# Performance work log

Hardware: AMD Instinct MI355X
Metric: run time of the kernel (lower is better)

## Reference

```python
import jax, jax.numpy as jnp
import numpy as np

H = 2048          # hidden_size
NH = 16           # num_attention_heads
D_NOPE = 64
D_ROPE = 64
D_V = 64
KV_RANK = 256
E = 8             # n_routed_experts
INTER = 1408      # moe_intermediate_size
EPS = 1e-6
THETA = 10000.0
B, S = 1, 2048
Q_HEAD = D_NOPE + D_ROPE


def rms_norm(x, w, eps=EPS):
    xf = x.astype(jnp.float32)
    var = jnp.mean(xf * xf, axis=-1, keepdims=True)
    return (w * (xf * jax.lax.rsqrt(var + eps))).astype(x.dtype)


def rotate_half(x):
    d = x.shape[-1] // 2
    return jnp.concatenate([-x[..., d:], x[..., :d]], axis=-1)


def rope_tables(seq_len, dim, theta=THETA):
    inv_freq = 1.0 / (theta ** (jnp.arange(0, dim, 2, dtype=jnp.float32) / dim))
    t = jnp.arange(seq_len, dtype=jnp.float32)
    freqs = jnp.outer(t, inv_freq)
    emb = jnp.concatenate([freqs, freqs], axis=-1)  # [S, dim]
    return jnp.cos(emb), jnp.sin(emb)


def setup_inputs() -> dict:
    key = jax.random.key(0)
    ks = jax.random.split(key, 10)
    sc = 0.02
    inp = {
        "positions": jnp.broadcast_to(jnp.arange(S, dtype=jnp.int32)[None, :], (B, S)),
        "hidden_states": jax.random.normal(ks[0], (B, S, H), dtype=jnp.float32),
        "input_ln_w": jnp.ones((H,), jnp.float32),
        "q_proj_w": jax.random.normal(ks[1], (NH * Q_HEAD, H), jnp.float32) * sc,
        "kv_a_w": jax.random.normal(ks[2], (KV_RANK + D_ROPE, H), jnp.float32) * sc,
        "kv_a_ln_w": jnp.ones((KV_RANK,), jnp.float32),
        "kv_b_w": jax.random.normal(ks[3], (NH * (D_NOPE + D_V), KV_RANK), jnp.float32) * sc,
        "o_proj_w": jax.random.normal(ks[4], (H, NH * D_V), jnp.float32) * sc,
        "post_ln_w": jnp.ones((H,), jnp.float32),
        "gate_w": jax.random.normal(ks[5], (E, H), jnp.float32) * sc,
        "fc1_w": jax.random.normal(ks[6], (E, INTER, H), jnp.float32) * sc,
        "fc2_w": jax.random.normal(ks[7], (E, H, INTER), jnp.float32) * sc,
    }
    return inp


def reference(positions, hidden_states, input_ln_w, q_proj_w, kv_a_w, kv_a_ln_w,
              kv_b_w, o_proj_w, post_ln_w, gate_w, fc1_w, fc2_w):
    x = hidden_states
    sa_in = rms_norm(x, input_ln_w)

    # Q projection -> [B, NH, S, D_NOPE + D_ROPE]
    q = (sa_in @ q_proj_w.T).reshape(B, S, NH, Q_HEAD).transpose(0, 2, 1, 3)
    q_nope, q_pe = q[..., :D_NOPE], q[..., D_NOPE:]

    # KV compression path
    ckv_pe = sa_in @ kv_a_w.T                       # [B, S, KV_RANK + D_ROPE]
    compressed_kv, k_pe = ckv_pe[..., :KV_RANK], ckv_pe[..., KV_RANK:]
    k_pe = k_pe.reshape(B, S, 1, D_ROPE).transpose(0, 2, 1, 3)  # [B,1,S,Dr]
    kv = (rms_norm(compressed_kv, kv_a_ln_w) @ kv_b_w.T)
    kv = kv.reshape(B, S, NH, D_NOPE + D_V).transpose(0, 2, 1, 3)
    k_nope, v = kv[..., :D_NOPE], kv[..., D_NOPE:]

    # RoPE on pe halves
    cos, sin = rope_tables(S, D_ROPE)
    cos_sel = cos[positions][:, None]               # [B,1,S,Dr]
    sin_sel = sin[positions][:, None]
    q_pe = q_pe * cos_sel + rotate_half(q_pe) * sin_sel
    k_pe = k_pe * cos_sel + rotate_half(k_pe) * sin_sel

    query = jnp.concatenate([q_nope, q_pe], axis=-1)                       # [B,NH,S,Dq]
    key = jnp.concatenate([k_nope, jnp.broadcast_to(k_pe, (B, NH, S, D_ROPE))], axis=-1)

    scale = Q_HEAD ** -0.5
    scores = jnp.einsum("bhqd,bhkd->bhqk", query, key) * scale
    causal = jnp.tril(jnp.ones((S, S), dtype=bool))
    scores = jnp.where(causal, scores, jnp.finfo(scores.dtype).min)
    attn = jax.nn.softmax(scores, axis=-1)
    ctx = jnp.einsum("bhqk,bhkd->bhqd", attn, v)                            # [B,NH,S,Dv]
    ctx = ctx.transpose(0, 2, 1, 3).reshape(B, S, NH * D_V)
    attn_out = ctx @ o_proj_w.T

    x = x + attn_out

    # dense all-expert MoE
    mlp_in = rms_norm(x, post_ln_w)
    probs = jax.nn.softmax(mlp_in @ gate_w.T, axis=-1)                      # [B,S,E]
    h = jax.nn.silu(jnp.einsum("bsd,eid->bsei", mlp_in, fc1_w))             # [B,S,E,INTER]
    moe_out = jnp.einsum("bse,bsei,ehi->bsh", probs, h, fc2_w)

    return x + moe_out
```

## Files before the change

### kernel.cpp

```cpp
#include <hip/hip_runtime.h>
#include <cstdint>
#include <cstddef>

typedef __bf16 bf16;
typedef __bf16 bf16x8 __attribute__((ext_vector_type(8)));
typedef float  f32x4  __attribute__((ext_vector_type(4)));

constexpr int S_      = 2048;
constexpr int H_      = 2048;
constexpr int NH_     = 16;
constexpr int KV_RANK_= 256;
constexpr int EXP_    = 8;
constexpr int INTER_  = 1408;
constexpr int QH_     = 128;
constexpr float EPS_  = 1e-6f;

__device__ inline void gload16(const void* g, void* l) {
  __builtin_amdgcn_global_load_lds(
      (const __attribute__((address_space(1))) void*)g,
      (__attribute__((address_space(3))) void*)l, 16, 0, 0);
}

enum { EPI_BF16 = 0, EPI_F32 = 1, EPI_ADD = 2, EPI_SILU = 3, EPI_ATOM = 4 };

template <int EPI, typename TB, int TILE>
__global__ void __launch_bounds__(256, 3) gemm_bt(
    const bf16* __restrict__ A, const TB* __restrict__ B,
    void* __restrict__ Cv, const float* __restrict__ aux,
    int M, int N, int K, int lda, int ldb, int ldc,
    long zA, long zB, long zC, long auxZ, int auxRS,
    int kPerE, long bExpStride, int expBasePerZ)
{
  constexpr int FR = TILE / 32;
  const int tileN = blockIdx.x * TILE;
  const int tileM = blockIdx.y * TILE;
  const int z = blockIdx.z;
  A += (long)z * zA;

  __shared__ __align__(16) bf16 As[TILE * 64];
  __shared__ __align__(16) TB   Bs[TILE * 64];
  char* AsB = (char*)As;
  char* BsB = (char*)Bs;

  const int tid  = threadIdx.x;
  const int lane = tid & 63;
  const int wave = tid >> 6;
  const int wr = wave >> 1, wc = wave & 1;
  const int quad = lane >> 4, r16 = lane & 15;

  const int ldbe = (kPerE > 0) ? kPerE : ldb;
  const TB* BzBase = (kPerE > 0) ? (B + (long)z * expBasePerZ * bExpStride)
                                 : (B + (long)z * zB);

  constexpr int IA = TILE / 32;
  const bf16* aG[IA]; char* aL[IA];
#pragma unroll
  for (int i = 0; i < IA; i++) {
    int n = (wave * IA + i) * 64 + lane;
    int row = n >> 3, cp = n & 7;
    int cc = (cp ^ (row & 7)) << 3;
    int rowg = tileM + row; if (rowg > M - 1) rowg = M - 1;
    aG[i] = A + (long)rowg * lda + cc;
    aL[i] = AsB + (long)(wave * IA + i) * 1024;
  }
  constexpr int IB = (sizeof(TB) == 4) ? (TILE / 16) : (TILE / 32);
  const TB* bG[IB]; char* bL[IB];
#pragma unroll
  for (int i = 0; i < IB; i++) {
    int n = (wave * IB + i) * 64 + lane;
    int row, cc;
    if constexpr (sizeof(TB) == 4) { row = n >> 4; cc = ((n & 15) ^ (row & 15)) << 2; }
    else                           { row = n >> 3; cc = ((n & 7)  ^ (row & 7))  << 3; }
    int rowg = tileN + row; if (rowg > N - 1) rowg = N - 1;
    bG[i] = BzBase + (long)rowg * ldbe + cc;
    bL[i] = BsB + (long)(wave * IB + i) * 1024;
  }

  int aOff[FR], bOff[FR];
#pragma unroll
  for (int i = 0; i < FR; i++) {
    int row = wr * (TILE / 2) + i * 16 + r16;
    aOff[i] = row * 128 + ((quad ^ (row & 7)) << 4);
  }
#pragma unroll
  for (int j = 0; j < FR; j++) {
    int row = wc * (TILE / 2) + j * 16 + r16;
    if constexpr (sizeof(TB) == 4) bOff[j] = row * 256 + (((2 * quad) ^ (row & 15)) << 4);
    else                           bOff[j] = row * 128 + ((quad ^ (row & 7)) << 4);
  }

  f32x4 acc[FR][FR];
#pragma unroll
  for (int i = 0; i < FR; i++)
#pragma unroll
    for (int j = 0; j < FR; j++)
#pragma unroll
      for (int r = 0; r < 4; r++) acc[i][j][r] = 0.f;

  int bk = 0; long eOff = 0;
  for (int k0 = 0; k0 < K; k0 += 64) {
#pragma unroll
    for (int i = 0; i < IA; i++) gload16(aG[i] + k0, aL[i]);
#pragma unroll
    for (int i = 0; i < IB; i++) gload16(bG[i] + eOff + bk, bL[i]);
    __syncthreads();

#pragma unroll
    for (int s = 0; s < 2; s++) {
      bf16x8 af[FR], bfv[FR];
#pragma unroll
      for (int i = 0; i < FR; i++)
        af[i] = *(const bf16x8*)(AsB + (aOff[i] ^ (s << 6)));
#pragma unroll
      for (int j = 0; j < FR; j++) {
        if constexpr (sizeof(TB) == 2) {
          bfv[j] = *(const bf16x8*)(BsB + (bOff[j] ^ (s << 6)));
        } else {
          int a0 = bOff[j] ^ (s << 7);
          f32x4 lo = *(const f32x4*)(BsB + a0);
          f32x4 hi = *(const f32x4*)(BsB + (a0 ^ 16));
          bf16x8 v;
          v[0]=(bf16)lo[0]; v[1]=(bf16)lo[1]; v[2]=(bf16)lo[2]; v[3]=(bf16)lo[3];
          v[4]=(bf16)hi[0]; v[5]=(bf16)hi[1]; v[6]=(bf16)hi[2]; v[7]=(bf16)hi[3];
          bfv[j] = v;
        }
      }
#pragma unroll
      for (int i = 0; i < FR; i++)
#pragma unroll
        for (int j = 0; j < FR; j++)
          acc[i][j] = __builtin_amdgcn_mfma_f32_16x16x32_bf16(af[i], bfv[j], acc[i][j], 0, 0, 0);
    }
    __syncthreads();

    bk += 64;
    if (kPerE > 0 && bk >= kPerE) { bk = 0; eOff += bExpStride; }
  }

  bf16*  Cb = (bf16*)Cv + (long)z * zC;
  float* Cf = (float*)Cv + (long)z * zC;
  const float* auxp = aux + (long)z * auxZ;
  const int mB = tileM + wr * (TILE / 2) + quad * 4;
  const int nB = tileN + wc * (TILE / 2) + r16;
#pragma unroll
  for (int i = 0; i < FR; i++) {
#pragma unroll
    for (int r = 0; r < 4; r++) {
      int gm = mB + i * 16 + r;
      if (gm >= M) continue;
      float rowAux = 0.f;
      if constexpr (EPI == EPI_SILU) rowAux = auxp[(long)gm * auxRS];
#pragma unroll
      for (int j = 0; j < FR; j++) {
        int gn = nB + j * 16;
        if (gn >= N) continue;
        float v = acc[i][j][r];
        long off = (long)gm * ldc + gn;
        if constexpr (EPI == EPI_BF16)      Cb[off] = (bf16)v;
        else if constexpr (EPI == EPI_F32)  Cf[off] = v;
        else if constexpr (EPI == EPI_ADD)  Cf[off] = auxp[(long)gm * auxRS + gn] + v;
        else if constexpr (EPI == EPI_SILU) { float sv = v / (1.f + __expf(-v)); Cb[off] = (bf16)(sv * rowAux); }
        else                                atomicAdd(&Cf[off], v);
      }
    }
  }
}

__global__ void __launch_bounds__(256) flash_k(
    const bf16* __restrict__ q, const bf16* __restrict__ k,
    const bf16* __restrict__ vt, bf16* __restrict__ ctx, float scale)
{
  const int h  = blockIdx.x;
  const int qt = (int)gridDim.y - 1 - (int)blockIdx.y;
  const int tid = threadIdx.x, lane = tid & 63, wave = tid >> 6;
  const int quad = lane >> 4, r16 = lane & 15;

  __shared__ __align__(16) bf16 Ks[64 * 128];
  __shared__ __align__(16) bf16 Vs[64 * 64];
  __shared__ __align__(16) bf16 Ps[4][16 * 64];
  char* KsB = (char*)Ks;
  char* VsB = (char*)Vs;
  char* PsB = (char*)&Ps[wave][0];

  bf16x8 qf[4];
  {
    const bf16* qp = q + ((long)h * S_ + qt * 64 + wave * 16 + r16) * 128 + quad * 8;
#pragma unroll
    for (int ks = 0; ks < 4; ks++) qf[ks] = *(const bf16x8*)(qp + ks * 32);
  }

  const bf16* kG[4]; char* kL[4];
#pragma unroll
  for (int i = 0; i < 4; i++) {
    int n = (wave * 4 + i) * 64 + lane;
    int row = n >> 4, c = n & 15;
    kG[i] = k + ((long)h * S_ + row) * 128 + ((c ^ (row & 15)) << 3);
    kL[i] = KsB + (long)(wave * 4 + i) * 1024;
  }
  const bf16* vG[2]; char* vL[2];
#pragma unroll
  for (int i = 0; i < 2; i++) {
    int n = (wave * 2 + i) * 64 + lane;
    int row = n >> 3, c = n & 7;
    vG[i] = vt + ((long)h * 64 + row) * S_ + ((c ^ (row & 7)) << 3);
    vL[i] = VsB + (long)(wave * 2 + i) * 1024;
  }

  float mr[4], lr[4];
#pragma unroll
  for (int r = 0; r < 4; r++) { mr[r] = -1e30f; lr[r] = 0.f; }
  f32x4 o[4];
#pragma unroll
  for (int j = 0; j < 4; j++)
#pragma unroll
    for (int r = 0; r < 4; r++) o[j][r] = 0.f;

  for (int kt = 0; kt <= qt; kt++) {
#pragma unroll
    for (int i = 0; i < 4; i++) gload16(kG[i] + (long)kt * 64 * 128, kL[i]);
#pragma unroll
    for (int i = 0; i < 2; i++) gload16(vG[i] + kt * 64, vL[i]);
    __syncthreads();

    f32x4 s[4];
#pragma unroll
    for (int j = 0; j < 4; j++)
#pragma unroll
      for (int r = 0; r < 4; r++) s[j][r] = 0.f;
#pragma unroll
    for (int ks = 0; ks < 4; ks++) {
#pragma unroll
      for (int j = 0; j < 4; j++) {
        int row = j * 16 + r16;
        int c = ks * 4 + quad;
        bf16x8 bfr = *(const bf16x8*)(KsB + row * 256 + ((c ^ (row & 15)) << 4));
        s[j] = __builtin_amdgcn_mfma_f32_16x16x32_bf16(qf[ks], bfr, s[j], 0, 0, 0);
      }
    }

    if (kt == qt) {
#pragma unroll
      for (int j = 0; j < 4; j++)
#pragma unroll
        for (int r = 0; r < 4; r++)
          if (j * 16 + r16 > wave * 16 + quad * 4 + r) s[j][r] = -1e30f;
    }

    float pj[4][4];
#pragma unroll
    for (int r = 0; r < 4; r++) {
      float mx = fmaxf(fmaxf(s[0][r], s[1][r]), fmaxf(s[2][r], s[3][r]));
#pragma unroll
      for (int off = 1; off < 16; off <<= 1) mx = fmaxf(mx, __shfl_xor(mx, off, 64));
      mx *= scale;
      float nm = fmaxf(mr[r], mx);
      float alpha = __expf(mr[r] - nm);
      mr[r] = nm;
      float rs = 0.f;
#pragma unroll
      for (int j = 0; j < 4; j++) { float e = __expf(s[j][r] * scale - nm); pj[j][r] = e; rs += e; }
#pragma unroll
      for (int off = 1; off < 16; off <<= 1) rs += __shfl_xor(rs, off, 64);
      lr[r] = lr[r] * alpha + rs;
#pragma unroll
      for (int j = 0; j < 4; j++) o[j][r] *= alpha;
    }

#pragma unroll
    for (int j = 0; j < 4; j++) {
      int chunk = j * 2 + (r16 >> 3);
#pragma unroll
      for (int r = 0; r < 4; r++) {
        int row = quad * 4 + r;
        *(bf16*)(PsB + row * 128 + ((chunk ^ (row & 7)) << 4) + ((r16 & 7) << 1)) = (bf16)pj[j][r];
      }
    }

#pragma unroll
    for (int ks = 0; ks < 2; ks++) {
      int c = ks * 4 + quad;
      bf16x8 af = *(const bf16x8*)(PsB + r16 * 128 + ((c ^ (r16 & 7)) << 4));
#pragma unroll
      for (int j = 0; j < 4; j++) {
        int row = j * 16 + r16;
        bf16x8 bfr = *(const bf16x8*)(VsB + row * 128 + ((c ^ (row & 7)) << 4));
        o[j] = __builtin_amdgcn_mfma_f32_16x16x32_bf16(af, bfr, o[j], 0, 0, 0);
      }
    }
    __syncthreads();
  }

  bf16* cp = ctx + ((long)(qt * 64 + wave * 16 + quad * 4)) * (NH_ * 64) + h * 64 + r16;
#pragma unroll
  for (int r = 0; r < 4; r++) {
    float rl = 1.f / lr[r];
#pragma unroll
    for (int j = 0; j < 4; j++)
      cp[(long)r * NH_ * 64 + j * 16] = (bf16)(o[j][r] * rl);
  }
}

template <int NIT>
__global__ void __launch_bounds__(256) rmsnorm_k(
    const float* __restrict__ x, const float* __restrict__ w,
    bf16* __restrict__ out, int inStride)
{
  const int row = blockIdx.x, tid = threadIdx.x;
  const float* xr = x + (long)row * inStride;
  float vals[NIT];
  float ss = 0.f;
#pragma unroll
  for (int i = 0; i < NIT; i++) { float v = xr[i * 256 + tid]; vals[i] = v; ss += v * v; }
#pragma unroll
  for (int o = 32; o; o >>= 1) ss += __shfl_xor(ss, o, 64);
  __shared__ float red[4];
  if ((tid & 63) == 0) red[tid >> 6] = ss;
  __syncthreads();
  ss = red[0] + red[1] + red[2] + red[3];
  const float rinv = rsqrtf(ss / (float)(NIT * 256) + EPS_);
  bf16* orow = out + (long)row * (NIT * 256);
#pragma unroll
  for (int i = 0; i < NIT; i++) { int c = i * 256 + tid; orow[c] = (bf16)(w[c] * vals[i] * rinv); }
}

__global__ void prep_qkv_k(const bf16* __restrict__ q, const bf16* __restrict__ kv,
                           const float* __restrict__ ckv, const int* __restrict__ pos,
                           bf16* __restrict__ query, bf16* __restrict__ key,
                           bf16* __restrict__ vvT)
{
  const int s = blockIdx.x, h = blockIdx.y, d = threadIdx.x;
  const long qkOff = ((long)h * S_ + s) * QH_ + d;
  if (d < 64) {
    query[qkOff] = q[(long)s * H_ + h * QH_ + d];
    key[qkOff]   = kv[(long)s * H_ + h * QH_ + d];
    vvT[((long)h * 64 + d) * S_ + s] = kv[(long)s * H_ + h * QH_ + 64 + d];
  } else {
    const int i = d - 64;
    const float p = (float)pos[s];
    const float invf = powf(10000.f, -(float)(2 * (i & 31)) / 64.f);
    const float ang = p * invf;
    const float cc = cosf(ang), sn = sinf(ang);
    const float xq  = (float)q[(long)s * H_ + h * QH_ + 64 + i];
    const float xqr = (i < 32) ? -(float)q[(long)s * H_ + h * QH_ + 64 + i + 32]
                               :  (float)q[(long)s * H_ + h * QH_ + 64 + i - 32];
    query[qkOff] = (bf16)(xq * cc + xqr * sn);
    const float xk  = ckv[(long)s * 320 + 256 + i];
    const float xkr = (i < 32) ? -ckv[(long)s * 320 + 256 + i + 32]
                               :  ckv[(long)s * 320 + 256 + i - 32];
    key[qkOff] = (bf16)(xk * cc + xkr * sn);
  }
}

__global__ void __launch_bounds__(256) gate_k(const bf16* __restrict__ mlp,
                                              const float* __restrict__ gw,
                                              float* __restrict__ probs)
{
  const int s = blockIdx.x, tid = threadIdx.x;
  float acc[8];
#pragma unroll
  for (int e = 0; e < 8; e++) acc[e] = 0.f;
  for (int c = tid; c < H_; c += 256) {
    float x = (float)mlp[(long)s * H_ + c];
#pragma unroll
    for (int e = 0; e < 8; e++) acc[e] += x * gw[e * H_ + c];
  }
  __shared__ float red[4][8];
#pragma unroll
  for (int e = 0; e < 8; e++) {
    float v = acc[e];
#pragma unroll
    for (int o = 32; o; o >>= 1) v += __shfl_xor(v, o, 64);
    if ((tid & 63) == 0) red[tid >> 6][e] = v;
  }
  __syncthreads();
  if (tid == 0) {
    float l[8]; float mx = -1e30f;
#pragma unroll
    for (int e = 0; e < 8; e++) { l[e] = red[0][e] + red[1][e] + red[2][e] + red[3][e]; mx = fmaxf(mx, l[e]); }
    float sum = 0.f;
#pragma unroll
    for (int e = 0; e < 8; e++) { l[e] = __expf(l[e] - mx); sum += l[e]; }
    float r = 1.f / sum;
#pragma unroll
    for (int e = 0; e < 8; e++) probs[(long)s * 8 + e] = l[e] * r;
  }
}

__global__ void __launch_bounds__(256) wconv_k(const float* __restrict__ in,
                                               bf16* __restrict__ out, int n8)
{
  int i = blockIdx.x * 256 + threadIdx.x;
  if (i < n8) {
    f32x4 a = ((const f32x4*)in)[2 * i];
    f32x4 b = ((const f32x4*)in)[2 * i + 1];
    bf16x8 v;
    v[0] = (bf16)a[0]; v[1] = (bf16)a[1]; v[2] = (bf16)a[2]; v[3] = (bf16)a[3];
    v[4] = (bf16)b[0]; v[5] = (bf16)b[1]; v[6] = (bf16)b[2]; v[7] = (bf16)b[3];
    ((bf16x8*)out)[i] = v;
  }
}

extern "C" void kernel_launch(void* const* d_in, const int* in_sizes, int n_in,
                              void* d_out, int out_size, void* d_ws, size_t ws_size,
                              hipStream_t stream)
{
  const int*   positions = (const int*)  d_in[0];
  const float* hidden    = (const float*)d_in[1];
  const float* ln1       = (const float*)d_in[2];
  const float* wq        = (const float*)d_in[3];
  const float* wkva      = (const float*)d_in[4];
  const float* lnkv      = (const float*)d_in[5];
  const float* wkvb      = (const float*)d_in[6];
  const float* wo        = (const float*)d_in[7];
  const float* ln2       = (const float*)d_in[8];
  const float* wg        = (const float*)d_in[9];
  const float* wfc1      = (const float*)d_in[10];
  const float* wfc2      = (const float*)d_in[11];
  float* out = (float*)d_out;

  char* wsb = (char*)d_ws;
  size_t off = 0;
  auto alloc = [&](size_t bytes) -> void* {
    void* p = wsb + off;
    off += (bytes + 255) & ~(size_t)255;
    return p;
  };
  bf16*  sa_in = (bf16*) alloc((size_t)S_ * H_ * 2);
  bf16*  qb    = (bf16*) alloc((size_t)S_ * H_ * 2);
  float* ckv   = (float*)alloc((size_t)S_ * 320 * 4);
  bf16*  ckvn  = (bf16*) alloc((size_t)S_ * KV_RANK_ * 2);
  bf16*  kvb   = (bf16*) alloc((size_t)S_ * H_ * 2);
  bf16*  query = (bf16*) alloc((size_t)NH_ * S_ * QH_ * 2);
  bf16*  key   = (bf16*) alloc((size_t)NH_ * S_ * QH_ * 2);
  bf16*  vvT   = (bf16*) alloc((size_t)NH_ * 64 * S_ * 2);
  bf16*  ctx   = (bf16*) alloc((size_t)S_ * NH_ * 64 * 2);
  bf16*  mlp   = (bf16*) alloc((size_t)S_ * H_ * 2);
  float* probs = (float*)alloc((size_t)S_ * 8 * 4);
  bf16*  hbuf  = (bf16*) alloc((size_t)S_ * EXP_ * INTER_ * 2);

  const size_t MBy = (size_t)1 << 20;
  const size_t rem = (ws_size > off) ? ws_size - off : 0;
  const size_t szMoeW = (size_t)EXP_ * INTER_ * H_ * 2;
  const bool cw = (rem >= 93 * MBy);

  bf16* fc1b = nullptr; bf16* fc2b = nullptr;
  if (cw) { fc1b = (bf16*)alloc(szMoeW); fc2b = (bf16*)alloc(szMoeW); }
  bf16* wqb   = (bf16*)hbuf;
  bf16* wkvab = wqb   + (size_t)H_ * H_;
  bf16* wkvbb = wkvab + (size_t)320 * H_;
  bf16* wob   = wkvbb + (size_t)H_ * KV_RANK_;

  const float scale = 0.08838834764831845f;

  rmsnorm_k<8><<<S_, 256, 0, stream>>>(hidden, ln1, sa_in, H_);

  if (cw) {
    wconv_k<<<(H_*H_/8 + 255)/256, 256, 0, stream>>>(wq, wqb, H_*H_/8);
    wconv_k<<<(320*H_/8 + 255)/256, 256, 0, stream>>>(wkva, wkvab, 320*H_/8);
    wconv_k<<<(H_*KV_RANK_/8 + 255)/256, 256, 0, stream>>>(wkvb, wkvbb, H_*KV_RANK_/8);
    wconv_k<<<(H_*NH_*64/8 + 255)/256, 256, 0, stream>>>(wo, wob, H_*NH_*64/8);
    wconv_k<<<(EXP_*INTER_*H_/8 + 255)/256, 256, 0, stream>>>(wfc1, fc1b, EXP_*INTER_*H_/8);
    wconv_k<<<(EXP_*INTER_*H_/8 + 255)/256, 256, 0, stream>>>(wfc2, fc2b, EXP_*INTER_*H_/8);
  }

  if (cw) gemm_bt<EPI_BF16, bf16, 64><<<dim3(32,32,1), 256, 0, stream>>>(
      sa_in, wqb, qb, hidden, S_, H_, H_, H_, H_, H_, 0,0,0,0,0, 0,0,0);
  else    gemm_bt<EPI_BF16, float, 64><<<dim3(32,32,1), 256, 0, stream>>>(
      sa_in, wq,  qb, hidden, S_, H_, H_, H_, H_, H_, 0,0,0,0,0, 0,0,0);

  if (cw) gemm_bt<EPI_F32, bf16, 64><<<dim3(5,32,1), 256, 0, stream>>>(
      sa_in, wkvab, ckv, hidden, S_, 320, H_, H_, H_, 320, 0,0,0,0,0, 0,0,0);
  else    gemm_bt<EPI_F32, float, 64><<<dim3(5,32,1), 256, 0, stream>>>(
      sa_in, wkva,  ckv, hidden, S_, 320, H_, H_, H_, 320, 0,0,0,0,0, 0,0,0);

  rmsnorm_k<1><<<S_, 256, 0, stream>>>(ckv, lnkv, ckvn, 320);

  if (cw) gemm_bt<EPI_BF16, bf16, 64><<<dim3(32,32,1), 256, 0, stream>>>(
      ckvn, wkvbb, kvb, hidden, S_, H_, KV_RANK_, KV_RANK_, KV_RANK_, H_, 0,0,0,0,0, 0,0,0);
  else    gemm_bt<EPI_BF16, float, 64><<<dim3(32,32,1), 256, 0, stream>>>(
      ckvn, wkvb,  kvb, hidden, S_, H_, KV_RANK_, KV_RANK_, KV_RANK_, H_, 0,0,0,0,0, 0,0,0);

  prep_qkv_k<<<dim3(S_, NH_), 128, 0, stream>>>(qb, kvb, ckv, positions, query, key, vvT);

  flash_k<<<dim3(NH_, S_/64), 256, 0, stream>>>(query, key, vvT, ctx, scale);

  if (cw) gemm_bt<EPI_ADD, bf16, 64><<<dim3(32,32,1), 256, 0, stream>>>(
      ctx, wob, out, hidden, S_, H_, NH_*64, NH_*64, NH_*64, H_, 0,0,0,0, H_, 0,0,0);
  else    gemm_bt<EPI_ADD, float, 64><<<dim3(32,32,1), 256, 0, stream>>>(
      ctx, wo,  out, hidden, S_, H_, NH_*64, NH_*64, NH_*64, H_, 0,0,0,0, H_, 0,0,0);

  rmsnorm_k<8><<<S_, 256, 0, stream>>>(out, ln2, mlp, H_);
  gate_k<<<S_, 256, 0, stream>>>(mlp, wg, probs);

  if (cw) gemm_bt<EPI_SILU, bf16, 128><<<dim3(11,16,8), 256, 0, stream>>>(
      mlp, fc1b, hbuf, probs, S_, INTER_, H_, H_, H_, EXP_*INTER_,
      0, (long)INTER_*H_, INTER_, 1, 8, 0, 0, 0);
  else    gemm_bt<EPI_SILU, float, 128><<<dim3(11,16,8), 256, 0, stream>>>(
      mlp, wfc1, hbuf, probs, S_, INTER_, H_, H_, H_, EXP_*INTER_,
      0, (long)INTER_*H_, INTER_, 1, 8, 0, 0, 0);

  if (cw) gemm_bt<EPI_ATOM, bf16, 128><<<dim3(16,16,8), 256, 0, stream>>>(
      hbuf, fc2b, out, hidden, S_, H_, INTER_, EXP_*INTER_, 0, H_,
      (long)INTER_, 0, 0, 0, 0, INTER_, (long)H_*INTER_, 1);
  else    gemm_bt<EPI_ATOM, float, 128><<<dim3(16,16,8), 256, 0, stream>>>(
      hbuf, wfc2, out, hidden, S_, H_, INTER_, EXP_*INTER_, 0, H_,
      (long)INTER_, 0, 0, 0, 0, INTER_, (long)H_*INTER_, 1);
}
```

Baseline: 751.3 us.

## Add 256x256 pipelined LDS-ring GEMM for MoE fc1/fc2 projections

Adds a new 512-thread GEMM kernel with 256x256 output tiles and an 8-slot LDS ring. Global-to-LDS loads for the next K step are interleaved with MFMA compute on the current step, using explicit barriers, vmcnt waits and setprio. fc1 is now one flat GEMM across all experts (N = 8*1408) instead of a per-expert z-batch. Both MoE GEMMs switch to this kernel when bf16 cached weights are present. The aim is more data reuse per tile and better latency hiding. The cost is about 128KB of LDS per block, which limits occupancy, and the hand-scheduled synchronisation is fragile.

Measured after the change: 767.8 us. +2.2%, slower.

```diff
diff --git a/kernel.cpp b/kernel.cpp
--- a/kernel.cpp
+++ b/kernel.cpp
@@ -20,6 +20,8 @@
       (const __attribute__((address_space(1))) void*)g,
       (__attribute__((address_space(3))) void*)l, 16, 0, 0);
 }
+
+#define CFENCE() asm volatile("" ::: "memory")
 
 enum { EPI_BF16 = 0, EPI_F32 = 1, EPI_ADD = 2, EPI_SILU = 3, EPI_ATOM = 4 };
 
@@ -161,6 +163,190 @@
         else if constexpr (EPI == EPI_ADD)  Cf[off] = auxp[(long)gm * auxRS + gn] + v;
         else if constexpr (EPI == EPI_SILU) { float sv = v / (1.f + __expf(-v)); Cb[off] = (bf16)(sv * rowAux); }
         else                                atomicAdd(&Cf[off], v);
+      }
+    }
+  }
+}
+
+template <int EPI>
+__global__ void __launch_bounds__(512, 2) gemm256_bt(
+    const bf16* __restrict__ A, const bf16* __restrict__ B,
+    void* __restrict__ Cv, const float* __restrict__ aux,
+    int K, int lda, int ldb, int ldc, long aZ, long bZ)
+{
+  const int tileN = blockIdx.x * 256;
+  const int tileM = blockIdx.y * 256;
+  const int z = blockIdx.z;
+  A += (long)z * aZ;
+  B += (long)z * bZ;
+
+  __shared__ __align__(16) bf16 ring[8 * 8192];
+  char* ringB = (char*)ring;
+
+  const int tid  = threadIdx.x;
+  const int lane = tid & 63;
+  const int wave = tid >> 6;
+  const int wr   = wave >> 2;
+  const int wc   = wave & 3;
+  const int quad = lane >> 4, r16 = lane & 15;
+
+  const bf16* aSrc[2][2];
+  const bf16* bSrc[2][2];
+#pragma unroll
+  for (int i = 0; i < 2; i++) {
+    int n = i * 512 + tid;
+    int row = n >> 3, cp = n & 7;
+    int cc = (cp ^ (row & 7)) << 3;
+#pragma unroll
+    for (int h = 0; h < 2; h++) {
+      aSrc[h][i] = A + (long)(tileM + h * 128 + row) * lda + cc;
+      bSrc[h][i] = B + (long)(tileN + h * 128 + row) * ldb + cc;
+    }
+  }
+  const int dstOff = tid * 16;
+
+  auto stageA = [&](int h, int kofs, int slot) {
+    gload16(aSrc[h][0] + kofs, ringB + slot * 16384 + dstOff);
+    gload16(aSrc[h][1] + kofs, ringB + slot * 16384 + 8192 + dstOff);
+  };
+  auto stageB = [&](int h, int kofs, int slot) {
+    gload16(bSrc[h][0] + kofs, ringB + slot * 16384 + dstOff);
+    gload16(bSrc[h][1] + kofs, ringB + slot * 16384 + 8192 + dstOff);
+  };
+
+  int aOffB[8], bOffB[4];
+#pragma unroll
+  for (int i = 0; i < 8; i++) {
+    int row = i * 16 + r16;
+    aOffB[i] = row * 128 + ((quad ^ (row & 7)) << 4);
+  }
+#pragma unroll
+  for (int j = 0; j < 4; j++) {
+    int row = (wc & 1) * 64 + j * 16 + r16;
+    bOffB[j] = row * 128 + ((quad ^ (row & 7)) << 4);
+  }
+  const char* aE = ringB + (2 + wr) * 16384;
+  const char* aO = ringB + (6 + wr) * 16384;
+  const char* bE = ringB + ((wc >> 1)) * 16384;
+  const char* bO = ringB + (4 + (wc >> 1)) * 16384;
+
+  f32x4 acc[8][4];
+#pragma unroll
+  for (int i = 0; i < 8; i++)
+#pragma unroll
+    for (int j = 0; j < 4; j++)
+#pragma unroll
+      for (int r = 0; r < 4; r++) acc[i][j][r] = 0.f;
+
+  stageB(0, 0, 0); stageB(1, 0, 1); stageA(0, 0, 2); stageA(1, 0, 3);
+  stageB(0, 64, 4); stageB(1, 64, 5);
+  asm volatile("s_waitcnt vmcnt(4)" ::: "memory");
+  CFENCE(); __builtin_amdgcn_s_barrier(); CFENCE();
+
+  const int NIT = K >> 7;
+  for (int it = 0; it < NIT; ++it) {
+    const bool last = (it == NIT - 1);
+    const int k1 = (2 * it + 1) << 6;
+    const int k2 = (2 * it + 2) << 6;
+    const int k3 = (2 * it + 3) << 6;
+    bf16x8 bfE[4][2], bfO[4][2];
+
+#pragma unroll
+    for (int q = 0; q < 4; ++q) {
+      bf16x8 af[2][2];
+#pragma unroll
+      for (int ii = 0; ii < 2; ++ii)
+#pragma unroll
+        for (int ks = 0; ks < 2; ++ks)
+          af[ii][ks] = *(const bf16x8*)(aE + (aOffB[2 * q + ii] ^ (ks << 6)));
+      if (q == 0) {
+#pragma unroll
+        for (int j = 0; j < 4; ++j)
+#pragma unroll
+          for (int ks = 0; ks < 2; ++ks)
+            bfE[j][ks] = *(const bf16x8*)(bE + (bOffB[j] ^ (ks << 6)));
+      }
+      if (q == 0)      stageA(0, k1, 6);
+      else if (q == 1) stageA(1, k1, 7);
+      else if (q == 2) { if (!last) stageB(0, k2, 0); }
+      else             { if (!last) stageB(1, k2, 1); }
+      CFENCE(); __builtin_amdgcn_s_barrier(); CFENCE();
+      __builtin_amdgcn_s_setprio(1);
+#pragma unroll
+      for (int ii = 0; ii < 2; ++ii)
+#pragma unroll
+        for (int ks = 0; ks < 2; ++ks)
+#pragma unroll
+          for (int j = 0; j < 4; ++j)
+            acc[2 * q + ii][j] = __builtin_amdgcn_mfma_f32_16x16x32_bf16(
+                af[ii][ks], bfE[j][ks], acc[2 * q + ii][j], 0, 0, 0);
+      __builtin_amdgcn_s_setprio(0);
+      if (q == 3) {
+        if (last) asm volatile("s_waitcnt vmcnt(0)" ::: "memory");
+        else      asm volatile("s_waitcnt vmcnt(4)" ::: "memory");
+      }
+      CFENCE(); __builtin_amdgcn_s_barrier(); CFENCE();
+    }
+
+#pragma unroll
+    for (int q = 0; q < 4; ++q) {
+      bf16x8 af[2][2];
+#pragma unroll
+      for (int ii = 0; ii < 2; ++ii)
+#pragma unroll
+        for (int ks = 0; ks < 2; ++ks)
+          af[ii][ks] = *(const bf16x8*)(aO + (aOffB[2 * q + ii] ^ (ks << 6)));
+      if (q == 0) {
+#pragma unroll
+        for (int j = 0; j < 4; ++j)
+#pragma unroll
+          for (int ks = 0; ks < 2; ++ks)
+            bfO[j][ks] = *(const bf16x8*)(bO + (bOffB[j] ^ (ks << 6)));
+      }
+      if (!last) {
+        if (q == 0)      stageA(0, k2, 2);
+        else if (q == 1) stageA(1, k2, 3);
+        else if (q == 2) stageB(0, k3, 4);
+        else             stageB(1, k3, 5);
+      }
+      CFENCE(); __builtin_amdgcn_s_barrier(); CFENCE();
+      __builtin_amdgcn_s_setprio(1);
+#pragma unroll
+      for (int ii = 0; ii < 2; ++ii)
+#pragma unroll
+        for (int ks = 0; ks < 2; ++ks)
+#pragma unroll
+          for (int j = 0; j < 4; ++j)
+            acc[2 * q + ii][j] = __builtin_amdgcn_mfma_f32_16x16x32_bf16(
+                af[ii][ks], bfO[j][ks], acc[2 * q + ii][j], 0, 0, 0);
+      __builtin_amdgcn_s_setprio(0);
+      if (q == 3 && !last) asm volatile("s_waitcnt vmcnt(4)" ::: "memory");
+      CFENCE(); __builtin_amdgcn_s_barrier(); CFENCE();
+    }
+  }
+
+  bf16*  Cb = (bf16*)Cv;
+  float* Cf = (float*)Cv;
+  const int mB = tileM + wr * 128 + quad * 4;
+  const int nB = tileN + wc * 64 + r16;
+#pragma unroll
+  for (int i = 0; i < 8; ++i) {
+#pragma unroll
+    for (int r = 0; r < 4; ++r) {
+      const int gm = mB + i * 16 + r;
+#pragma unroll
+      for (int j = 0; j < 4; ++j) {
+        const int gn = nB + j * 16;
+        float v = acc[i][j][r];
+        long off = (long)gm * ldc + gn;
+        if constexpr (EPI == EPI_SILU) {
+          float sv = v / (1.f + __expf(-v));
+          Cb[off] = (bf16)(sv * aux[(long)gm * 8 + (gn / INTER_)]);
+        } else if constexpr (EPI == EPI_ATOM) {
+          atomicAdd(&Cf[off], v);
+        } else {
+          Cb[off] = (bf16)v;
+        }
       }
     }
   }
@@ -492,17 +678,18 @@
   rmsnorm_k<8><<<S_, 256, 0, stream>>>(out, ln2, mlp, H_);
   gate_k<<<S_, 256, 0, stream>>>(mlp, wg, probs);
 
-  if (cw) gemm_bt<EPI_SILU, bf16, 128><<<dim3(11,16,8), 256, 0, stream>>>(
-      mlp, fc1b, hbuf, probs, S_, INTER_, H_, H_, H_, EXP_*INTER_,
-      0, (long)INTER_*H_, INTER_, 1, 8, 0, 0, 0);
-  else    gemm_bt<EPI_SILU, float, 128><<<dim3(11,16,8), 256, 0, stream>>>(
-      mlp, wfc1, hbuf, probs, S_, INTER_, H_, H_, H_, EXP_*INTER_,
-      0, (long)INTER_*H_, INTER_, 1, 8, 0, 0, 0);
-
-  if (cw) gemm_bt<EPI_ATOM, bf16, 128><<<dim3(16,16,8), 256, 0, stream>>>(
-      hbuf, fc2b, out, hidden, S_, H_, INTER_, EXP_*INTER_, 0, H_,
-      (long)INTER_, 0, 0, 0, 0, INTER_, (long)H_*INTER_, 1);
-  else    gemm_bt<EPI_ATOM, float, 128><<<dim3(16,16,8), 256, 0, stream>>>(
-      hbuf, wfc2, out, hidden, S_, H_, INTER_, EXP_*INTER_, 0, H_,
-      (long)INTER_, 0, 0, 0, 0, INTER_, (long)H_*INTER_, 1);
-}
+  if (cw) {
+    gemm256_bt<EPI_SILU><<<dim3(44, 8, 1), 512, 0, stream>>>(
+        mlp, fc1b, hbuf, probs, H_, H_, H_, EXP_*INTER_, 0, 0);
+    gemm256_bt<EPI_ATOM><<<dim3(8, 8, 8), 512, 0, stream>>>(
+        hbuf, fc2b, out, nullptr, INTER_, EXP_*INTER_, INTER_, H_,
+        (long)INTER_, (long)H_*INTER_);
+  } else {
+    gemm_bt<EPI_SILU, float, 128><<<dim3(11,16,8), 256, 0, stream>>>(
+        mlp, wfc1, hbuf, probs, S_, INTER_, H_, H_, H_, EXP_*INTER_,
+        0, (long)INTER_*H_, INTER_, 1, 8, 0, 0, 0);
+    gemm_bt<EPI_ATOM, float, 128><<<dim3(16,16,8), 256, 0, stream>>>(
+        hbuf, wfc2, out, hidden, S_, H_, INTER_, EXP_*INTER_, 0, H_,
+        (long)INTER_, 0, 0, 0, 0, INTER_, (long)H_*INTER_, 1);
+  }
+}
```
